# Kernel optimization log

Hardware: AMD Instinct MI355X
Metric: run time of the kernel (lower is better)

The kernel has to match this reference:

```python
import jax, jax.numpy as jnp
import numpy as np

NEG_SLOPE = 0.01  # torch nn.LeakyReLU default
N_NODES, N_EDGES, N_BATCH, L_PATH = 100000, 300000, 50000, 4
D_EMB, D_HID, N_HEADS = 128, 64, 8


def setup_inputs() -> dict:
    key = jax.random.key(0)
    ks = jax.random.split(key, 10)
    return {
        "batch_nodes": jax.random.randint(ks[0], (N_BATCH,), 0, N_NODES),
        "metapath_indices": jax.random.randint(ks[1], (N_EDGES, L_PATH), 0, N_NODES),
        "edge_dst": jax.random.randint(ks[2], (N_EDGES,), 0, N_NODES),
        "transformed_feature": jax.random.normal(ks[3], (N_NODES, D_EMB), jnp.float32),
        "W_i": jax.random.normal(ks[4], (D_HID, D_EMB), jnp.float32) * 0.05,
        "W_p": jax.random.normal(ks[5], (D_HID, D_EMB), jnp.float32) * 0.05,
        "attn": jax.random.normal(ks[6], (1, N_HEADS, D_HID), jnp.float32) * 0.05,
        "W_th": jax.random.normal(ks[7], (N_HEADS, N_HEADS), jnp.float32) * 0.3,
        "W_gate": jax.random.normal(ks[8], (1, D_HID), jnp.float32) * 0.1,
        "b_gate": jnp.zeros((1,), jnp.float32),
    }


def reference(batch_nodes, metapath_indices, edge_dst, transformed_feature,
              W_i, W_p, attn, W_th, W_gate, b_gate):
    N = transformed_feature.shape[0]
    # node_type_specific_agg for mtype==1: h_src/h_dst through linear_i, h_p1/h_p2 through linear_p
    membd = transformed_feature[metapath_indices]                      # [E, 4, D_emb]
    edata = (membd[:, 0] + membd[:, 3]) @ W_i.T \
          + (membd[:, 1] + membd[:, 2]) @ W_p.T                        # [E, D]
    E, D = edata.shape
    H = attn.shape[1]
    # cat([edata]*H, dim=1).view(-1, H, D) duplicates edata per head
    efeat = jnp.broadcast_to(edata[:, None, :], (E, H, D))             # [E, H, D]
    # talking-heads attention logits, leaky-relu
    logits = (efeat * attn).sum(-1) @ W_th.T                           # [E, H]
    logits = jax.nn.leaky_relu(logits, NEG_SLOPE)
    # dgl edge_softmax: per-dst-node, per-head softmax over incoming edges (stable)
    m = jax.ops.segment_max(logits, edge_dst, num_segments=N)          # [N, H]
    ex = jnp.exp(logits - m[edge_dst])                                 # [E, H]
    den = jax.ops.segment_sum(ex, edge_dst, num_segments=N)            # [N, H]
    a = ex / den[edge_dst]                                             # [E, H]  (dropout rate 0)
    # message passing: ft = efeature * a, summed per dst node
    msgs = (efeat * a[:, :, None]).reshape(E, H * D)
    node_ft = jax.ops.segment_sum(msgs, edge_dst, num_segments=N)      # [N, H*D]
    result = node_ft[batch_nodes].reshape(-1, H, D)                    # [B, H, D]
    # gated multi-head attention: gate = mean over batch of fc_gate(result)
    gate = jnp.mean(result @ W_gate.T + b_gate, axis=0)                # [H, 1]
    result = result * gate[None]                                       # [B, H, D]
    return result.reshape(-1, H * D)
```

## Files before the change

### kernel.cpp

```cpp
#include <hip/hip_runtime.h>
#include <cstdint>
#include <cstddef>


typedef __attribute__((ext_vector_type(8))) short bf16x8;
typedef __attribute__((ext_vector_type(4))) float f32x4;

__device__ __forceinline__ unsigned short f2bf(float f) {
    unsigned u = __float_as_uint(f);
    unsigned r = u + 0x7fffu + ((u >> 16) & 1u);
    return (unsigned short)(r >> 16);
}
__device__ __forceinline__ float bf2f(unsigned short h) {
    return __uint_as_float((unsigned)h << 16);
}

__global__ __launch_bounds__(256) void k_prepW(
    const float* __restrict__ Wi, const float* __restrict__ Wp,
    unsigned short* __restrict__ Whi, unsigned short* __restrict__ Wlo) {
    int t = blockIdx.x * 256 + threadIdx.x;
    if (t >= 16384) return;
    int j = t & 7, L = (t >> 3) & 63, c = (t >> 9) & 7, s = t >> 12;
    int k = s * 32 + (L >> 4) * 8 + j;
    int n = c * 16 + (L & 15);
    float v = (n < 64) ? Wi[n * 128 + k] : Wp[(n - 64) * 128 + k];
    unsigned short h = f2bf(v);
    Whi[t] = h;
    Wlo[t] = f2bf(v - bf2f(h));
}

__global__ __launch_bounds__(256) void k_dense(
    const float* __restrict__ feat, const unsigned short* __restrict__ Whi,
    const unsigned short* __restrict__ Wlo, unsigned short* __restrict__ Ybf, int M) {
    int wave = threadIdx.x >> 6;
    int L = threadIdx.x & 63;
    int m = L & 15, q = L >> 4;
    int R0 = blockIdx.x * 64 + wave * 16;

    f32x4 acc[8];
#pragma unroll
    for (int c = 0; c < 8; ++c) acc[c] = (f32x4){0.f, 0.f, 0.f, 0.f};

    int rowc = R0 + m; if (rowc > M - 1) rowc = M - 1;
    const float* arow = feat + (size_t)rowc * 128;

    for (int s = 0; s < 4; ++s) {
        const float4* ap = (const float4*)(arow + s * 32 + q * 8);
        float4 a0 = ap[0], a1 = ap[1];
        float av[8] = {a0.x, a0.y, a0.z, a0.w, a1.x, a1.y, a1.z, a1.w};
        bf16x8 ahi, alo;
#pragma unroll
        for (int j = 0; j < 8; ++j) {
            unsigned short h = f2bf(av[j]);
            ahi[j] = (short)h;
            alo[j] = (short)f2bf(av[j] - bf2f(h));
        }
#pragma unroll
        for (int c = 0; c < 8; ++c) {
            const bf16x8 bh = *(const bf16x8*)(Whi + ((s * 8 + c) * 512 + L * 8));
            const bf16x8 bl = *(const bf16x8*)(Wlo + ((s * 8 + c) * 512 + L * 8));
            acc[c] = __builtin_amdgcn_mfma_f32_16x16x32_bf16(ahi, bh, acc[c], 0, 0, 0);
            acc[c] = __builtin_amdgcn_mfma_f32_16x16x32_bf16(ahi, bl, acc[c], 0, 0, 0);
            acc[c] = __builtin_amdgcn_mfma_f32_16x16x32_bf16(alo, bh, acc[c], 0, 0, 0);
        }
    }
#pragma unroll
    for (int c = 0; c < 8; ++c) {
#pragma unroll
        for (int r = 0; r < 4; ++r) {
            int row = R0 + q * 4 + r;
            if (row < M) Ybf[(size_t)row * 128 + c * 16 + m] = f2bf(acc[c][r]);
        }
    }
}

__global__ __launch_bounds__(256) void k_P(
    const unsigned short* __restrict__ Ybf, const float* __restrict__ attn,
    float* __restrict__ P, int N) {
    int n = blockIdx.x * 4 + (threadIdx.x >> 6);
    int lane = threadIdx.x & 63;
    if (n >= N) return;
    const unsigned short* yr = Ybf + (size_t)n * 128;
    float y0 = bf2f(yr[2 * lane]), y1 = bf2f(yr[2 * lane + 1]);
    int d0 = (2 * lane) & 63, d1 = (2 * lane + 1) & 63;
#pragma unroll
    for (int i = 0; i < 8; ++i) {
        float p = y0 * attn[i * 64 + d0] + y1 * attn[i * 64 + d1];
#pragma unroll
        for (int o = 1; o < 32; o <<= 1) p += __shfl_xor(p, o);
        if (lane == 0)  P[n * 16 + i] = p;
        if (lane == 32) P[n * 16 + 8 + i] = p;
    }
}

__global__ __launch_bounds__(256) void k_count(
    const int* __restrict__ batch_nodes, int* __restrict__ mult, int B) {
    int i = blockIdx.x * 256 + threadIdx.x;
    if (i < B) atomicAdd(&mult[batch_nodes[i]], 1);
}

__global__ __launch_bounds__(256) void k_hist(
    const int* __restrict__ edge_dst, const int* __restrict__ mult,
    int* __restrict__ count, int E) {
    int e = blockIdx.x * 256 + threadIdx.x;
    if (e >= E) return;
    int d = edge_dst[e];
    if (mult[d] > 0) atomicAdd(&count[d], 1);
}

__global__ __launch_bounds__(256) void k_scan1(
    const int* __restrict__ count, int* __restrict__ excl, int* __restrict__ partials, int N) {
    __shared__ int lds[256];
    int t = threadIdx.x, i = blockIdx.x * 256 + t;
    int c = (i < N) ? count[i] : 0;
    lds[t] = c; __syncthreads();
    for (int o = 1; o < 256; o <<= 1) {
        int v = (t >= o) ? lds[t - o] : 0;
        __syncthreads(); lds[t] += v; __syncthreads();
    }
    if (i < N) excl[i] = lds[t] - c;
    if (t == 255) partials[blockIdx.x] = lds[255];
}
__global__ __launch_bounds__(512) void k_scan2(
    const int* __restrict__ partials, int* __restrict__ blockoff,
    int* __restrict__ offsets, int nb, int N) {
    __shared__ int lds[512];
    int t = threadIdx.x;
    int c = (t < nb) ? partials[t] : 0;
    lds[t] = c; __syncthreads();
    for (int o = 1; o < 512; o <<= 1) {
        int v = (t >= o) ? lds[t - o] : 0;
        __syncthreads(); lds[t] += v; __syncthreads();
    }
    if (t < nb) blockoff[t] = lds[t] - c;
    if (t == nb - 1) offsets[N] = lds[t];
}
__global__ __launch_bounds__(256) void k_scan3(
    const int* __restrict__ excl, const int* __restrict__ blockoff,
    int* __restrict__ offsets, int* __restrict__ cursor, int N) {
    int i = blockIdx.x * 256 + threadIdx.x;
    if (i < N) {
        int o = excl[i] + blockoff[i >> 8];
        offsets[i] = o; cursor[i] = o;
    }
}

__global__ __launch_bounds__(256) void k_scatter(
    const int* __restrict__ edge_dst, const int* __restrict__ mult,
    int* __restrict__ cursor, int* __restrict__ csr, int E) {
    int e = blockIdx.x * 256 + threadIdx.x;
    if (e >= E) return;
    int d = edge_dst[e];
    if (mult[d] > 0) {
        int pos = atomicAdd(&cursor[d], 1);
        csr[pos] = e;
    }
}

__global__ __launch_bounds__(256) void k_logits(
    const int* __restrict__ csr, const int* __restrict__ pEc,
    const int* __restrict__ mp, const float* __restrict__ P,
    const float* __restrict__ Wth, float* __restrict__ logits,
    int4* __restrict__ mpc) {
    int Ec = *pEc;
    int i = blockIdx.x * 32 + (threadIdx.x >> 3);
    if (i >= Ec) return;
    int h = threadIdx.x & 7;
    int e = csr[i];
    int4 rows = *(const int4*)(mp + (size_t)e * 4);
    float s = P[rows.x * 16 + h] + P[rows.w * 16 + h]
            + P[rows.y * 16 + 8 + h] + P[rows.z * 16 + 8 + h];
    int gbase = threadIdx.x & ~7;
    float l = 0.f;
#pragma unroll
    for (int j = 0; j < 8; ++j) {
        float sj = __shfl(s, gbase + j);
        l += Wth[h * 8 + j] * sj;
    }
    l = l > 0.f ? l : 0.01f * l;
    logits[(size_t)i * 8 + h] = l;
    if (h == 0) mpc[i] = rows;
}

__global__ __launch_bounds__(256) void k_node_agg(
    const unsigned short* __restrict__ Ybf, const float* __restrict__ logits,
    const int4* __restrict__ mpc, const int* __restrict__ offsets,
    const int* __restrict__ mult, const float* __restrict__ Wg,
    unsigned short* __restrict__ nftb, float* __restrict__ gate_part, int N) {
    int n = blockIdx.x * 4 + (threadIdx.x >> 6);
    int lane = threadIdx.x & 63;
    if (n >= N) return;
    int m = mult[n];
    if (m == 0) return;
    int beg = offsets[n], end = offsets[n + 1];

    float mx[8];
#pragma unroll
    for (int h = 0; h < 8; ++h) mx[h] = -1e30f;
    for (int j = beg; j < end; ++j) {
        const float4* lp = (const float4*)(logits + (size_t)j * 8);
        float4 l0 = lp[0], l1 = lp[1];
        mx[0] = fmaxf(mx[0], l0.x); mx[1] = fmaxf(mx[1], l0.y);
        mx[2] = fmaxf(mx[2], l0.z); mx[3] = fmaxf(mx[3], l0.w);
        mx[4] = fmaxf(mx[4], l1.x); mx[5] = fmaxf(mx[5], l1.y);
        mx[6] = fmaxf(mx[6], l1.z); mx[7] = fmaxf(mx[7], l1.w);
    }
    float den[8], acc[8];
#pragma unroll
    for (int h = 0; h < 8; ++h) { den[h] = 0.f; acc[h] = 0.f; }
    for (int j = beg; j < end; ++j) {
        const float4* lp = (const float4*)(logits + (size_t)j * 8);
        float4 l0 = lp[0], l1 = lp[1];
        int4 rows = mpc[j];
        float ed = bf2f(Ybf[(size_t)rows.x * 128 + lane])
                 + bf2f(Ybf[(size_t)rows.w * 128 + lane])
                 + bf2f(Ybf[(size_t)rows.y * 128 + 64 + lane])
                 + bf2f(Ybf[(size_t)rows.z * 128 + 64 + lane]);
        float w0 = __expf(l0.x - mx[0]), w1 = __expf(l0.y - mx[1]);
        float w2 = __expf(l0.z - mx[2]), w3 = __expf(l0.w - mx[3]);
        float w4 = __expf(l1.x - mx[4]), w5 = __expf(l1.y - mx[5]);
        float w6 = __expf(l1.z - mx[6]), w7 = __expf(l1.w - mx[7]);
        den[0] += w0; den[1] += w1; den[2] += w2; den[3] += w3;
        den[4] += w4; den[5] += w5; den[6] += w6; den[7] += w7;
        acc[0] += w0 * ed; acc[1] += w1 * ed; acc[2] += w2 * ed; acc[3] += w3 * ed;
        acc[4] += w4 * ed; acc[5] += w5 * ed; acc[6] += w6 * ed; acc[7] += w7 * ed;
    }
#pragma unroll
    for (int h = 0; h < 8; ++h) {
        float r = (end > beg) ? 1.f / den[h] : 0.f;
        acc[h] *= r;
    }

    unsigned short* base = nftb + (size_t)n * 512;
#pragma unroll
    for (int h = 0; h < 8; ++h) base[h * 64 + lane] = f2bf(acc[h]);

    float wg = Wg[lane];
    float myg = 0.f;
#pragma unroll
    for (int h = 0; h < 8; ++h) {
        float p = acc[h] * wg;
#pragma unroll
        for (int o = 32; o > 0; o >>= 1) p += __shfl_xor(p, o);
        if (lane == h) myg = p;
    }
    if (lane < 8)
        atomicAdd(&gate_part[(blockIdx.x & 1023) * 8 + lane], (float)m * myg);
}

__global__ __launch_bounds__(256) void k_gatefinal(
    const float* __restrict__ gate_part, const float* __restrict__ b_gate,
    float* __restrict__ gate, int B) {
    __shared__ float lds[256];
    int t = threadIdx.x;
    int h = t & 7, g = t >> 3;
    float s = 0.f;
    for (int b = g; b < 1024; b += 32) s += gate_part[b * 8 + h];
    lds[t] = s; __syncthreads();
    if (t < 8) {
        float tot = 0.f;
        for (int gg = 0; gg < 32; ++gg) tot += lds[gg * 8 + t];
        gate[t] = tot / (float)B + b_gate[0];
    }
}

__global__ __launch_bounds__(256) void k_output(
    const unsigned short* __restrict__ nftb, const int* __restrict__ batch_nodes,
    const float* __restrict__ gate, float* __restrict__ out, int B) {
    int idx = blockIdx.x * 256 + threadIdx.x;
    int total = B * 128;
    if (idx >= total) return;
    int b = idx >> 7;
    int rem4 = idx & 127;
    int h = rem4 >> 4;
    int n = batch_nodes[b];
    ushort4 v = *(const ushort4*)(nftb + (size_t)n * 512 + rem4 * 4);
    float g = gate[h];
    float4 o;
    o.x = bf2f(v.x) * g; o.y = bf2f(v.y) * g;
    o.z = bf2f(v.z) * g; o.w = bf2f(v.w) * g;
    *(float4*)(out + (size_t)idx * 4) = o;
}

extern "C" void kernel_launch(void* const* d_in, const int* in_sizes, int n_in,
                              void* d_out, int out_size, void* d_ws, size_t ws_size,
                              hipStream_t stream) {
    const int*   batch_nodes = (const int*)d_in[0];
    const int*   mp          = (const int*)d_in[1];
    const int*   edge_dst    = (const int*)d_in[2];
    const float* feat        = (const float*)d_in[3];
    const float* W_i         = (const float*)d_in[4];
    const float* W_p         = (const float*)d_in[5];
    const float* attn        = (const float*)d_in[6];
    const float* W_th        = (const float*)d_in[7];
    const float* W_gate      = (const float*)d_in[8];
    const float* b_gate      = (const float*)d_in[9];
    float* out = (float*)d_out;

    const int B = in_sizes[0];
    const int E = in_sizes[2];
    const int N = in_sizes[3] / 128;
    const int nb_scan = (N + 255) / 256;

    char* w = (char*)d_ws;
    auto alloc = [&](size_t bytes) -> void* {
        void* p = (void*)w;
        w += (bytes + 255) & ~(size_t)255;
        return p;
    };
    unsigned short* Whi = (unsigned short*)alloc(16384 * 2);
    unsigned short* Wlo = (unsigned short*)alloc(16384 * 2);
    unsigned short* Ybf = (unsigned short*)alloc((size_t)N * 128 * 2);
    float* P            = (float*)alloc((size_t)N * 16 * 4);
    float* logits       = (float*)alloc((size_t)E * 8 * 4);
    int4*  mpc          = (int4*)alloc((size_t)E * 16);
    int*   mult         = (int*)alloc((size_t)N * 4);
    int*   count        = (int*)alloc((size_t)N * 4);
    int*   excl         = (int*)alloc((size_t)N * 4);
    int*   offsets      = (int*)alloc((size_t)(N + 1) * 4);
    int*   cursor       = (int*)alloc((size_t)N * 4);
    int*   partials     = (int*)alloc(512 * 4);
    int*   blockoff     = (int*)alloc(512 * 4);
    int*   csr          = (int*)alloc((size_t)E * 4);
    unsigned short* nftb = (unsigned short*)alloc((size_t)N * 512 * 2);
    float* gate_part    = (float*)alloc(1024 * 8 * 4);
    float* gate         = (float*)alloc(256);

    hipMemsetAsync(mult, 0, (size_t)N * 4, stream);
    hipMemsetAsync(count, 0, (size_t)N * 4, stream);
    hipMemsetAsync(gate_part, 0, 1024 * 8 * 4, stream);

    k_prepW<<<64, 256, 0, stream>>>(W_i, W_p, Whi, Wlo);
    k_dense<<<(N + 63) / 64, 256, 0, stream>>>(feat, Whi, Wlo, Ybf, N);
    k_P<<<(N + 3) / 4, 256, 0, stream>>>(Ybf, attn, P, N);

    k_count<<<(B + 255) / 256, 256, 0, stream>>>(batch_nodes, mult, B);
    k_hist<<<(E + 255) / 256, 256, 0, stream>>>(edge_dst, mult, count, E);
    k_scan1<<<nb_scan, 256, 0, stream>>>(count, excl, partials, N);
    k_scan2<<<1, 512, 0, stream>>>(partials, blockoff, offsets, nb_scan, N);
    k_scan3<<<nb_scan, 256, 0, stream>>>(excl, blockoff, offsets, cursor, N);
    k_scatter<<<(E + 255) / 256, 256, 0, stream>>>(edge_dst, mult, cursor, csr, E);

    const int* pEc = offsets + N;
    k_logits<<<(E + 31) / 32, 256, 0, stream>>>(csr, pEc, mp, P, W_th, logits, mpc);
    k_node_agg<<<(N + 3) / 4, 256, 0, stream>>>(Ybf, logits, mpc, offsets, mult,
                                                W_gate, nftb, gate_part, N);
    k_gatefinal<<<1, 256, 0, stream>>>(gate_part, b_gate, gate, B);
    k_output<<<(B * 128 + 255) / 256, 256, 0, stream>>>(nftb, batch_nodes, gate, out, B);
}
```

Baseline: 363.1 us.

## Fuse projection with attention dot, compact edges, and compute logits with online softmax

Folds the per-node attention projection P into the dense MFMA kernel through an LDS staging buffer, and merges the batch-node counting with the weight prep kernel while building a compacted list of flagged nodes. The histogram pass records kept edges so the scatter only touches those and stores metapath rows directly in CSR order. Logit computation moves into the aggregation kernel, which uses an online softmax and launches only over flagged nodes rather than all nodes. This removes several launches and the logits and mpc buffers. In exchange it adds global atomic counters, extra LDS use in the dense kernel, and more exp work per edge.

```diff
diff --git a/kernel.cpp b/kernel.cpp
--- a/kernel.cpp
+++ b/kernel.cpp
@@ -15,25 +15,44 @@
     return __uint_as_float((unsigned)h << 16);
 }
 
-__global__ __launch_bounds__(256) void k_prepW(
+__global__ __launch_bounds__(256) void k_prep(
     const float* __restrict__ Wi, const float* __restrict__ Wp,
-    unsigned short* __restrict__ Whi, unsigned short* __restrict__ Wlo) {
-    int t = blockIdx.x * 256 + threadIdx.x;
-    if (t >= 16384) return;
-    int j = t & 7, L = (t >> 3) & 63, c = (t >> 9) & 7, s = t >> 12;
-    int k = s * 32 + (L >> 4) * 8 + j;
-    int n = c * 16 + (L & 15);
-    float v = (n < 64) ? Wi[n * 128 + k] : Wp[(n - 64) * 128 + k];
-    unsigned short h = f2bf(v);
-    Whi[t] = h;
-    Wlo[t] = f2bf(v - bf2f(h));
+    unsigned short* __restrict__ Whi, unsigned short* __restrict__ Wlo,
+    const int* __restrict__ batch_nodes, int* __restrict__ mult,
+    int* __restrict__ flagged, int* __restrict__ nf, int B) {
+    if (blockIdx.x < 64) {
+        int t = blockIdx.x * 256 + threadIdx.x;
+        int j = t & 7, L = (t >> 3) & 63, c = (t >> 9) & 7, s = t >> 12;
+        int k = s * 32 + (L >> 4) * 8 + j;
+        int n = c * 16 + (L & 15);
+        float v = (n < 64) ? Wi[n * 128 + k] : Wp[(n - 64) * 128 + k];
+        unsigned short h = f2bf(v);
+        Whi[t] = h;
+        Wlo[t] = f2bf(v - bf2f(h));
+    } else {
+        int i = (int)(blockIdx.x - 64) * 256 + threadIdx.x;
+        if (i < B) {
+            int n = batch_nodes[i];
+            if (atomicAdd(&mult[n], 1) == 0) {
+                int p = atomicAdd(nf, 1);
+                flagged[p] = n;
+            }
+        }
+    }
 }
 
 __global__ __launch_bounds__(256) void k_dense(
     const float* __restrict__ feat, const unsigned short* __restrict__ Whi,
-    const unsigned short* __restrict__ Wlo, unsigned short* __restrict__ Ybf, int M) {
-    int wave = threadIdx.x >> 6;
-    int L = threadIdx.x & 63;
+    const unsigned short* __restrict__ Wlo, const float* __restrict__ attn,
+    unsigned short* __restrict__ Ybf, float* __restrict__ P, int M) {
+    __shared__ float sY[64 * 132];
+    __shared__ float sAt[512];
+    int t = threadIdx.x;
+    sAt[t] = attn[t];
+    sAt[256 + t] = attn[256 + t];
+
+    int wave = t >> 6;
+    int L = t & 63;
     int m = L & 15, q = L >> 4;
     int R0 = blockIdx.x * 64 + wave * 16;
 
@@ -68,44 +87,49 @@
     for (int c = 0; c < 8; ++c) {
 #pragma unroll
         for (int r = 0; r < 4; ++r) {
+            int lrow = wave * 16 + q * 4 + r;
             int row = R0 + q * 4 + r;
+            sY[lrow * 132 + c * 16 + m] = acc[c][r];
             if (row < M) Ybf[(size_t)row * 128 + c * 16 + m] = f2bf(acc[c][r]);
         }
     }
-}
-
-__global__ __launch_bounds__(256) void k_P(
-    const unsigned short* __restrict__ Ybf, const float* __restrict__ attn,
-    float* __restrict__ P, int N) {
-    int n = blockIdx.x * 4 + (threadIdx.x >> 6);
-    int lane = threadIdx.x & 63;
-    if (n >= N) return;
-    const unsigned short* yr = Ybf + (size_t)n * 128;
-    float y0 = bf2f(yr[2 * lane]), y1 = bf2f(yr[2 * lane + 1]);
-    int d0 = (2 * lane) & 63, d1 = (2 * lane + 1) & 63;
-#pragma unroll
-    for (int i = 0; i < 8; ++i) {
-        float p = y0 * attn[i * 64 + d0] + y1 * attn[i * 64 + d1];
-#pragma unroll
-        for (int o = 1; o < 32; o <<= 1) p += __shfl_xor(p, o);
-        if (lane == 0)  P[n * 16 + i] = p;
-        if (lane == 32) P[n * 16 + 8 + i] = p;
-    }
-}
-
-__global__ __launch_bounds__(256) void k_count(
-    const int* __restrict__ batch_nodes, int* __restrict__ mult, int B) {
-    int i = blockIdx.x * 256 + threadIdx.x;
-    if (i < B) atomicAdd(&mult[batch_nodes[i]], 1);
+    __syncthreads();
+
+    if (t < 128) {
+        int row = t >> 1, half = t & 1;
+        int g = blockIdx.x * 64 + row;
+        if (g < M) {
+            float p[8];
+#pragma unroll
+            for (int i = 0; i < 8; ++i) p[i] = 0.f;
+            const float* yr = &sY[row * 132 + half * 64];
+#pragma unroll 4
+            for (int k4 = 0; k4 < 16; ++k4) {
+                float4 y = *(const float4*)(yr + k4 * 4);
+#pragma unroll
+                for (int i = 0; i < 8; ++i) {
+                    const float* a = &sAt[i * 64 + k4 * 4];
+                    p[i] += y.x * a[0] + y.y * a[1] + y.z * a[2] + y.w * a[3];
+                }
+            }
+#pragma unroll
+            for (int i = 0; i < 8; ++i) P[(size_t)g * 16 + half * 8 + i] = p[i];
+        }
+    }
 }
 
 __global__ __launch_bounds__(256) void k_hist(
     const int* __restrict__ edge_dst, const int* __restrict__ mult,
-    int* __restrict__ count, int E) {
+    int* __restrict__ count, int2* __restrict__ kept, int* __restrict__ keptCnt,
+    int E) {
     int e = blockIdx.x * 256 + threadIdx.x;
     if (e >= E) return;
     int d = edge_dst[e];
-    if (mult[d] > 0) atomicAdd(&count[d], 1);
+    if (mult[d] > 0) {
+        atomicAdd(&count[d], 1);
+        int p = atomicAdd(keptCnt, 1);
+        kept[p] = make_int2(e, d);
+    }
 }
 
 __global__ __launch_bounds__(256) void k_scan1(
@@ -146,103 +170,81 @@
 }
 
 __global__ __launch_bounds__(256) void k_scatter(
-    const int* __restrict__ edge_dst, const int* __restrict__ mult,
-    int* __restrict__ cursor, int* __restrict__ csr, int E) {
-    int e = blockIdx.x * 256 + threadIdx.x;
-    if (e >= E) return;
-    int d = edge_dst[e];
-    if (mult[d] > 0) {
-        int pos = atomicAdd(&cursor[d], 1);
-        csr[pos] = e;
-    }
-}
-
-__global__ __launch_bounds__(256) void k_logits(
-    const int* __restrict__ csr, const int* __restrict__ pEc,
-    const int* __restrict__ mp, const float* __restrict__ P,
-    const float* __restrict__ Wth, float* __restrict__ logits,
-    int4* __restrict__ mpc) {
-    int Ec = *pEc;
-    int i = blockIdx.x * 32 + (threadIdx.x >> 3);
-    if (i >= Ec) return;
-    int h = threadIdx.x & 7;
-    int e = csr[i];
-    int4 rows = *(const int4*)(mp + (size_t)e * 4);
-    float s = P[rows.x * 16 + h] + P[rows.w * 16 + h]
-            + P[rows.y * 16 + 8 + h] + P[rows.z * 16 + 8 + h];
-    int gbase = threadIdx.x & ~7;
-    float l = 0.f;
-#pragma unroll
-    for (int j = 0; j < 8; ++j) {
-        float sj = __shfl(s, gbase + j);
-        l += Wth[h * 8 + j] * sj;
-    }
-    l = l > 0.f ? l : 0.01f * l;
-    logits[(size_t)i * 8 + h] = l;
-    if (h == 0) mpc[i] = rows;
-}
-
-__global__ __launch_bounds__(256) void k_node_agg(
-    const unsigned short* __restrict__ Ybf, const float* __restrict__ logits,
-    const int4* __restrict__ mpc, const int* __restrict__ offsets,
-    const int* __restrict__ mult, const float* __restrict__ Wg,
-    unsigned short* __restrict__ nftb, float* __restrict__ gate_part, int N) {
-    int n = blockIdx.x * 4 + (threadIdx.x >> 6);
+    const int2* __restrict__ kept, const int* __restrict__ keptCnt,
+    const int4* __restrict__ mp4, int* __restrict__ cursor,
+    int4* __restrict__ csrmp) {
+    int i = blockIdx.x * 256 + threadIdx.x;
+    if (i >= *keptCnt) return;
+    int2 kd = kept[i];
+    int4 rows = mp4[kd.x];
+    int pos = atomicAdd(&cursor[kd.y], 1);
+    csrmp[pos] = rows;
+}
+
+__global__ __launch_bounds__(256) void k_agg(
+    const unsigned short* __restrict__ Ybf, const float* __restrict__ P,
+    const int4* __restrict__ csrmp, const int* __restrict__ offsets,
+    const int* __restrict__ flagged, const int* __restrict__ nf,
+    const int* __restrict__ mult, const float* __restrict__ Wth,
+    const float* __restrict__ Wg, unsigned short* __restrict__ nftb,
+    float* __restrict__ gate_part) {
+    int wid = blockIdx.x * 4 + (threadIdx.x >> 6);
     int lane = threadIdx.x & 63;
-    if (n >= N) return;
+    if (wid >= *nf) return;
+    int n = flagged[wid];
     int m = mult[n];
-    if (m == 0) return;
     int beg = offsets[n], end = offsets[n + 1];
-
-    float mx[8];
-#pragma unroll
-    for (int h = 0; h < 8; ++h) mx[h] = -1e30f;
+    int h = lane & 7;
+
+    float wth[8];
+#pragma unroll
+    for (int j = 0; j < 8; ++j) wth[j] = Wth[h * 8 + j];
+
+    float mx[8], den[8], acc[8];
+#pragma unroll
+    for (int i = 0; i < 8; ++i) { mx[i] = -1e30f; den[i] = 0.f; acc[i] = 0.f; }
+
     for (int j = beg; j < end; ++j) {
-        const float4* lp = (const float4*)(logits + (size_t)j * 8);
-        float4 l0 = lp[0], l1 = lp[1];
-        mx[0] = fmaxf(mx[0], l0.x); mx[1] = fmaxf(mx[1], l0.y);
-        mx[2] = fmaxf(mx[2], l0.z); mx[3] = fmaxf(mx[3], l0.w);
-        mx[4] = fmaxf(mx[4], l1.x); mx[5] = fmaxf(mx[5], l1.y);
-        mx[6] = fmaxf(mx[6], l1.z); mx[7] = fmaxf(mx[7], l1.w);
-    }
-    float den[8], acc[8];
-#pragma unroll
-    for (int h = 0; h < 8; ++h) { den[h] = 0.f; acc[h] = 0.f; }
-    for (int j = beg; j < end; ++j) {
-        const float4* lp = (const float4*)(logits + (size_t)j * 8);
-        float4 l0 = lp[0], l1 = lp[1];
-        int4 rows = mpc[j];
+        int4 rows = csrmp[j];
+        float s = P[(size_t)rows.x * 16 + h] + P[(size_t)rows.w * 16 + h]
+                + P[(size_t)rows.y * 16 + 8 + h] + P[(size_t)rows.z * 16 + 8 + h];
+        float l = 0.f;
+#pragma unroll
+        for (int jj = 0; jj < 8; ++jj) l += wth[jj] * __shfl(s, jj);
+        l = l > 0.f ? l : 0.01f * l;
         float ed = bf2f(Ybf[(size_t)rows.x * 128 + lane])
                  + bf2f(Ybf[(size_t)rows.w * 128 + lane])
                  + bf2f(Ybf[(size_t)rows.y * 128 + 64 + lane])
                  + bf2f(Ybf[(size_t)rows.z * 128 + 64 + lane]);
-        float w0 = __expf(l0.x - mx[0]), w1 = __expf(l0.y - mx[1]);
-        float w2 = __expf(l0.z - mx[2]), w3 = __expf(l0.w - mx[3]);
-        float w4 = __expf(l1.x - mx[4]), w5 = __expf(l1.y - mx[5]);
-        float w6 = __expf(l1.z - mx[6]), w7 = __expf(l1.w - mx[7]);
-        den[0] += w0; den[1] += w1; den[2] += w2; den[3] += w3;
-        den[4] += w4; den[5] += w5; den[6] += w6; den[7] += w7;
-        acc[0] += w0 * ed; acc[1] += w1 * ed; acc[2] += w2 * ed; acc[3] += w3 * ed;
-        acc[4] += w4 * ed; acc[5] += w5 * ed; acc[6] += w6 * ed; acc[7] += w7 * ed;
-    }
-#pragma unroll
-    for (int h = 0; h < 8; ++h) {
-        float r = (end > beg) ? 1.f / den[h] : 0.f;
-        acc[h] *= r;
+#pragma unroll
+        for (int hh = 0; hh < 8; ++hh) {
+            float lh = __shfl(l, hh);
+            float m2 = fmaxf(mx[hh], lh);
+            float sc = __expf(mx[hh] - m2);
+            float w = __expf(lh - m2);
+            den[hh] = den[hh] * sc + w;
+            acc[hh] = acc[hh] * sc + w * ed;
+            mx[hh] = m2;
+        }
+    }
+#pragma unroll
+    for (int i = 0; i < 8; ++i) {
+        float r = (end > beg) ? 1.f / den[i] : 0.f;
+        acc[i] *= r;
     }
 
     unsigned short* base = nftb + (size_t)n * 512;
 #pragma unroll
-    for (int h = 0; h < 8; ++h) base[h * 64 + lane] = f2bf(acc[h]);
+    for (int i = 0; i < 8; ++i) base[i * 64 + lane] = f2bf(acc[i]);
 
     float wg = Wg[lane];
     float myg = 0.f;
 #pragma unroll
-    for (int h = 0; h < 8; ++h) {
-        float p = acc[h] * wg;
+    for (int i = 0; i < 8; ++i) {
+        float p = acc[i] * wg;
 #pragma unroll
         for (int o = 32; o > 0; o >>= 1) p += __shfl_xor(p, o);
-        if (lane == h) myg = p;
+        if (lane == i) myg = p;
     }
     if (lane < 8)
         atomicAdd(&gate_part[(blockIdx.x & 1023) * 8 + lane], (float)m * myg);
@@ -308,43 +310,41 @@
         w += (bytes + 255) & ~(size_t)255;
         return p;
     };
+    size_t zbytes = (size_t)N * 4 + (size_t)N * 4 + 8192 * 4 + 256;
+    char* zb            = (char*)alloc(zbytes);
+    int*   mult         = (int*)zb;
+    int*   count        = (int*)(zb + (size_t)N * 4);
+    float* gate_part    = (float*)(zb + 2 * (size_t)N * 4);
+    int*   nf           = (int*)(zb + 2 * (size_t)N * 4 + 8192 * 4);
+    int*   keptCnt      = nf + 1;
+
     unsigned short* Whi = (unsigned short*)alloc(16384 * 2);
     unsigned short* Wlo = (unsigned short*)alloc(16384 * 2);
     unsigned short* Ybf = (unsigned short*)alloc((size_t)N * 128 * 2);
     float* P            = (float*)alloc((size_t)N * 16 * 4);
-    float* logits       = (float*)alloc((size_t)E * 8 * 4);
-    int4*  mpc          = (int4*)alloc((size_t)E * 16);
-    int*   mult         = (int*)alloc((size_t)N * 4);
-    int*   count        = (int*)alloc((size_t)N * 4);
+    int*   flagged      = (int*)alloc((size_t)N * 4);
+    int2*  kept         = (int2*)alloc((size_t)E * 8);
     int*   excl         = (int*)alloc((size_t)N * 4);
     int*   offsets      = (int*)alloc((size_t)(N + 1) * 4);
     int*   cursor       = (int*)alloc((size_t)N * 4);
     int*   partials     = (int*)alloc(512 * 4);
     int*   blockoff     = (int*)alloc(512 * 4);
-    int*   csr          = (int*)alloc((size_t)E * 4);
+    int4*  csrmp        = (int4*)alloc((size_t)E * 16);
     unsigned short* nftb = (unsigned short*)alloc((size_t)N * 512 * 2);
-    float* gate_part    = (float*)alloc(1024 * 8 * 4);
     float* gate         = (float*)alloc(256);
 
-    hipMemsetAsync(mult, 0, (size_t)N * 4, stream);
-    hipMemsetAsync(count, 0, (size_t)N * 4, stream);
-    hipMemsetAsync(gate_part, 0, 1024 * 8 * 4, stream);
-
-    k_prepW<<<64, 256, 0, stream>>>(W_i, W_p, Whi, Wlo);
-    k_dense<<<(N + 63) / 64, 256, 0, stream>>>(feat, Whi, Wlo, Ybf, N);
-    k_P<<<(N + 3) / 4, 256, 0, stream>>>(Ybf, attn, P, N);
-
-    k_count<<<(B + 255) / 256, 256, 0, stream>>>(batch_nodes, mult, B);
-    k_hist<<<(E + 255) / 256, 256, 0, stream>>>(edge_dst, mult, count, E);
+    hipMemsetAsync(zb, 0, zbytes, stream);
+
+    k_prep<<<64 + (B + 255) / 256, 256, 0, stream>>>(
+        W_i, W_p, Whi, Wlo, batch_nodes, mult, flagged, nf, B);
+    k_dense<<<(N + 63) / 64, 256, 0, stream>>>(feat, Whi, Wlo, attn, Ybf, P, N);
+    k_hist<<<(E + 255) / 256, 256, 0, stream>>>(edge_dst, mult, count, kept, keptCnt, E);
     k_scan1<<<nb_scan, 256, 0, stream>>>(count, excl, partials, N);
     k_scan2<<<1, 512, 0, stream>>>(partials, blockoff, offsets, nb_scan, N);
     k_scan3<<<nb_scan, 256, 0, stream>>>(excl, blockoff, offsets, cursor, N);
-    k_scatter<<<(E + 255) / 256, 256, 0, stream>>>(edge_dst, mult, cursor, csr, E);
-
-    const int* pEc = offsets + N;
-    k_logits<<<(E + 31) / 32, 256, 0, stream>>>(csr, pEc, mp, P, W_th, logits, mpc);
-    k_node_agg<<<(N + 3) / 4, 256, 0, stream>>>(Ybf, logits, mpc, offsets, mult,
-                                                W_gate, nftb, gate_part, N);
+    k_scatter<<<(E + 255) / 256, 256, 0, stream>>>(kept, keptCnt, (const int4*)mp, cursor, csrmp);
+    k_agg<<<(B + 3) / 4, 256, 0, stream>>>(Ybf, P, csrmp, offsets, flagged, nf,
+                                           mult, W_th, W_gate, nftb, gate_part);
     k_gatefinal<<<1, 256, 0, stream>>>(gate_part, b_gate, gate, B);
     k_output<<<(B * 128 + 255) / 256, 256, 0, stream>>>(nftb, batch_nodes, gate, out, B);
 }
```

Result: slower. 375.1 us (+3.3%).
